# Kernel tuning notes

Measured on AMD Instinct MI355X. Metric: run time of the kernel, lower is better.

## Reference

```python
import jax, jax.numpy as jnp
import numpy as np

N = 100000; E = 1000000; D = 192; FD = 64; L = 6; MLP = 192
TW = 768; NPD = 6; CPD = 7; TEMP = 0.5; NREL = 2; EPS = 1e-5


def _ln(x, g, b):
    mu = jnp.mean(x, axis=-1, keepdims=True)
    var = jnp.mean(jnp.square(x - mu), axis=-1, keepdims=True)
    return (x - mu) * jax.lax.rsqrt(var + EPS) * g + b


def _bn(x, g, b):
    # BatchNorm1d in training mode: batch statistics over the N (node) axis
    mu = jnp.mean(x, axis=0, keepdims=True)
    var = jnp.mean(jnp.square(x - mu), axis=0, keepdims=True)
    return (x - mu) * jax.lax.rsqrt(var + EPS) * g + b


def _rgcn(x, Wrel, Wroot, bias, src, dst, etype):
    # PyG RGCNConv, aggr='mean': out_i = x_i @ Wroot + b + sum_r mean_{j in N_r(i)} x_j @ W_r
    out = x @ Wroot + bias
    for r in range(NREL):
        h = x @ Wrel[r]                                   # [N, D] per-relation transform
        mask = (etype == r)
        msg = jnp.where(mask[:, None], jnp.take(h, src, axis=0), 0.0)  # [E, D]
        agg = jax.ops.segment_sum(msg, dst, num_segments=N)
        cnt = jax.ops.segment_sum(mask.astype(x.dtype), dst, num_segments=N)
        out = out + agg / jnp.maximum(cnt, 1.0)[:, None]
    return out


def _forward(tweet, num_prop, comments_prop,
             Wt, bt, Wn, bnum, Wc, bc,
             Wv, bv, Wo, bo, ln1_g, ln1_b, bn_g, bn_b,
             W1, b1, W2, b2, ln2_g, ln2_b,
             Wrel, Wroot, rgcn_b, Wm1, bm1, Wm2, bm2, Wm3, bm3,
             edge_index, edge_type, labels, train_idx):
    lrelu = jax.nn.leaky_relu  # negative_slope=0.01, same as torch LeakyReLU default
    t = lrelu(tweet @ Wt + bt)
    n = lrelu(num_prop @ Wn + bnum)
    c = lrelu(comments_prop @ Wc + bc)
    x = jnp.concatenate([t, n, c], axis=1)  # [N, D]; seq dim of size 1 is elided
    for i in range(L):
        # MHA over seq_len=1: softmax over a single key is exactly 1, so
        # attn_out = out_proj(v_proj(x)); Q/K projections have zero effect/grad.
        v = x @ Wv[i] + bv[i]
        x = x + (v @ Wo[i] + bo[i])          # dropout in eval mode = identity
        x = _ln(x, ln1_g[i], ln1_b[i])
        x = _bn(x, bn_g[i], bn_b[i])
        f = lrelu(x @ W1[i] + b1[i]) @ W2[i] + b2[i]
        x = x + f
        x = _ln(x, ln2_g[i], ln2_b[i])
    # supervised contrastive loss on first train_idx nodes (train_idx static int)
    feat = x[:train_idx]
    lab = labels[:train_idx]
    fn = feat / jnp.linalg.norm(feat, axis=-1, keepdims=True)
    sim = (fn @ fn.T) / TEMP                              # [T, T]
    ex = jnp.exp(sim)
    match = (lab[:, None] == lab[None, :]).astype(x.dtype)
    closs = jnp.mean(-jnp.log(jnp.sum(match * ex, axis=1) / jnp.sum(ex, axis=1)))
    # two passes through the SAME (shared-weight) RGCN; dropout(p=0.1) eval = identity
    src, dst = edge_index[0], edge_index[1]
    h = _rgcn(x, Wrel, Wroot, rgcn_b, src, dst, edge_type)
    h = _rgcn(h, Wrel, Wroot, rgcn_b, src, dst, edge_type)
    h = lrelu(h @ Wm1 + bm1)
    h = lrelu(h @ Wm2 + bm2)
    logits = h @ Wm3 + bm3                                # [N, 2]
    return logits, closs


def setup_inputs() -> dict:
    key = jax.random.key(0)
    ks = iter(jax.random.split(key, 64))
    f32 = jnp.float32
    def p(*shape):
        fan_in = shape[-2] if len(shape) >= 2 else shape[-1]
        return jax.random.normal(next(ks), shape, f32) * (1.0 / np.sqrt(fan_in))
    inp = {
        'tweet': jax.random.normal(next(ks), (N, TW), f32),
        'num_prop': jax.random.normal(next(ks), (N, NPD), f32),
        'comments_prop': jax.random.normal(next(ks), (N, CPD), f32),
        'Wt': p(TW, FD), 'bt': jnp.zeros((FD,), f32),
        'Wn': p(NPD, FD), 'bnum': jnp.zeros((FD,), f32),
        'Wc': p(CPD, FD), 'bc': jnp.zeros((FD,), f32),
        'Wv': p(L, D, D), 'bv': jnp.zeros((L, D), f32),
        'Wo': p(L, D, D), 'bo': jnp.zeros((L, D), f32),
        'ln1_g': jnp.ones((L, D), f32), 'ln1_b': jnp.zeros((L, D), f32),
        'bn_g': jnp.ones((L, D), f32), 'bn_b': jnp.zeros((L, D), f32),
        'W1': p(L, D, MLP), 'b1': jnp.zeros((L, MLP), f32),
        'W2': p(L, MLP, D), 'b2': jnp.zeros((L, D), f32),
        'ln2_g': jnp.ones((L, D), f32), 'ln2_b': jnp.zeros((L, D), f32),
        'Wrel': p(NREL, D, D), 'Wroot': p(D, D), 'rgcn_b': jnp.zeros((D,), f32),
        'Wm1': p(D, MLP), 'bm1': jnp.zeros((MLP,), f32),
        'Wm2': p(MLP, D), 'bm2': jnp.zeros((D,), f32),
        'Wm3': p(D, 2), 'bm3': jnp.zeros((2,), f32),
        'edge_index': jax.random.randint(next(ks), (2, E), 0, N, jnp.int32),
        'edge_type': jax.random.randint(next(ks), (E,), 0, NREL, jnp.int32),
        'labels': jax.random.randint(next(ks), (N,), 0, 2, jnp.int32),
        'train_idx': 8192,
    }
    return inp


def reference(tweet, num_prop, comments_prop, Wt, bt, Wn, bnum, Wc, bc,
              Wv, bv, Wo, bo, ln1_g, ln1_b, bn_g, bn_b,
              W1, b1, W2, b2, ln2_g, ln2_b,
              Wrel, Wroot, rgcn_b, Wm1, bm1, Wm2, bm2, Wm3, bm3,
              edge_index, edge_type, labels, train_idx):
    return _forward(tweet, num_prop, comments_prop, Wt, bt, Wn, bnum, Wc, bc,
                    Wv, bv, Wo, bo, ln1_g, ln1_b, bn_g, bn_b,
                    W1, b1, W2, b2, ln2_g, ln2_b,
                    Wrel, Wroot, rgcn_b, Wm1, bm1, Wm2, bm2, Wm3, bm3,
                    edge_index, edge_type, labels, train_idx)
```

## Files before the change

kernel.cpp:

```cpp
#include <hip/hip_runtime.h>

#define NN 100000
#define EE 1000000
#define DDIM 192
#define NLAYER 6
#define TRAIN 8192
#define SLOPE 0.01f
#define EPS_LN 1e-5f
#define TOTSEG (2 * NN)
#define SCAN_NB 98

typedef float f32x4 __attribute__((ext_vector_type(4)));
typedef __bf16 bf16x8 __attribute__((ext_vector_type(8)));
typedef unsigned short ushort_t;
typedef unsigned int uint_t;

__device__ __forceinline__ float lrelu(float v) { return v > 0.0f ? v : SLOPE * v; }

__device__ __forceinline__ ushort_t f2bf(float f) {
    union { float f; uint_t u; } v; v.f = f;
    uint_t u = v.u;
    u += 0x7fffu + ((u >> 16) & 1u);
    return (ushort_t)(u >> 16);
}

__device__ __forceinline__ float bf2f(ushort_t b) {
    union { uint_t u; float f; } v; v.u = ((uint_t)b) << 16; return v.f;
}

__device__ __forceinline__ float wave_sum(float s) {
    #pragma unroll
    for (int off = 32; off > 0; off >>= 1) s += __shfl_down(s, off);
    return __shfl(s, 0);
}

__global__ __launch_bounds__(256) void prep_w(
    const float* __restrict__ Wt, const float* __restrict__ Wv,
    const float* __restrict__ Wo, const float* __restrict__ W1,
    const float* __restrict__ W2, const float* __restrict__ Wrel,
    const float* __restrict__ Wroot, const float* __restrict__ Wm1,
    const float* __restrict__ Wm2, ushort_t* __restrict__ WTt,
    ushort_t* __restrict__ WTs, ushort_t* __restrict__ WTg)
{
    const int bid = blockIdx.x;
    if (bid < 29 * 144) {
        const int mat = bid / 144;
        const int o = (bid % 144) * 256 + threadIdx.x;
        const float* src;
        if      (mat <  6) src = Wv   + (size_t)mat * 36864;
        else if (mat < 12) src = Wo   + (size_t)(mat - 6)  * 36864;
        else if (mat < 18) src = W1   + (size_t)(mat - 12) * 36864;
        else if (mat < 24) src = W2   + (size_t)(mat - 18) * 36864;
        else if (mat < 26) src = Wrel + (size_t)(mat - 24) * 36864;
        else if (mat == 26) src = Wroot;
        else if (mat == 27) src = Wm1;
        else                src = Wm2;
        const int m = o / 192, k = o - m * 192;
        const ushort_t b = f2bf(src[(size_t)k * 192 + m]);
        if (mat == 24 || mat == 25)
            WTg[(size_t)m * 576 + 192 + (mat - 24) * 192 + k] = b;
        else if (mat == 26)
            WTg[(size_t)m * 576 + k] = b;
        else
            WTs[(size_t)mat * 36864 + o] = b;
    } else {
        const int o = (bid - 29 * 144) * 256 + threadIdx.x;
        const int m = o / 768, k = o - m * 768;
        WTt[o] = f2bf(Wt[(size_t)k * 64 + m]);
    }
}

template <int NFRAG, bool BIAS, bool RELU>
__global__ __launch_bounds__(256) void gemm_mfma(
    const float* __restrict__ A, const ushort_t* __restrict__ WT,
    const float* __restrict__ bias, float* __restrict__ C,
    int n, int K, int ldc)
{
    __shared__ ushort_t As[128 * 32];
    __shared__ ushort_t Ws[NFRAG * 16 * 32];
    const int tid = threadIdx.x;
    const int lane = tid & 63, w = tid >> 6;
    const int quad = lane >> 4, l15 = lane & 15;
    const int row0 = blockIdx.x * 128;

    f32x4 acc[2][NFRAG];
    #pragma unroll
    for (int m = 0; m < 2; ++m)
        #pragma unroll
        for (int nf = 0; nf < NFRAG; ++nf)
            acc[m][nf] = (f32x4){0.f, 0.f, 0.f, 0.f};

    const int srow = tid >> 1, shalf = tid & 1;
    const bool arow_ok = (row0 + srow) < n;
    const float* aptr = A + (size_t)(row0 + srow) * K + shalf * 16;
    const int ktiles = K >> 5;

    float f[16];
    if (arow_ok) {
        const float4* p = (const float4*)aptr;
        #pragma unroll
        for (int i = 0; i < 4; ++i) {
            const float4 t4 = p[i];
            f[i * 4 + 0] = t4.x; f[i * 4 + 1] = t4.y;
            f[i * 4 + 2] = t4.z; f[i * 4 + 3] = t4.w;
        }
    } else {
        #pragma unroll
        for (int i = 0; i < 16; ++i) f[i] = 0.f;
    }

    for (int t = 0; t < ktiles; ++t) {
        const int k0 = t << 5;
        uint_t u[8];
        #pragma unroll
        for (int i = 0; i < 8; ++i)
            u[i] = (uint_t)f2bf(f[2 * i]) | ((uint_t)f2bf(f[2 * i + 1]) << 16);
        uint4* dsta = (uint4*)&As[srow * 32 + shalf * 16];
        dsta[0] = make_uint4(u[0], u[1], u[2], u[3]);
        dsta[1] = make_uint4(u[4], u[5], u[6], u[7]);

        #pragma unroll
        for (int s = tid; s < NFRAG * 64; s += 256) {
            const int col = s >> 2, part = s & 3;
            *(uint4*)&Ws[col * 32 + part * 8] =
                *(const uint4*)(WT + (size_t)col * K + k0 + part * 8);
        }
        __syncthreads();

        float fn_[16];
        const bool more = (t + 1 < ktiles);
        if (more) {
            if (arow_ok) {
                const float4* p = (const float4*)(aptr + k0 + 32);
                #pragma unroll
                for (int i = 0; i < 4; ++i) {
                    const float4 t4 = p[i];
                    fn_[i * 4 + 0] = t4.x; fn_[i * 4 + 1] = t4.y;
                    fn_[i * 4 + 2] = t4.z; fn_[i * 4 + 3] = t4.w;
                }
            } else {
                #pragma unroll
                for (int i = 0; i < 16; ++i) fn_[i] = 0.f;
            }
        }

        const bf16x8 a0 = *(const bf16x8*)&As[(w * 32 + l15) * 32 + quad * 8];
        const bf16x8 a1 = *(const bf16x8*)&As[(w * 32 + 16 + l15) * 32 + quad * 8];
        #pragma unroll
        for (int nf = 0; nf < NFRAG; ++nf) {
            const bf16x8 b = *(const bf16x8*)&Ws[(nf * 16 + l15) * 32 + quad * 8];
            acc[0][nf] = __builtin_amdgcn_mfma_f32_16x16x32_bf16(a0, b, acc[0][nf], 0, 0, 0);
            acc[1][nf] = __builtin_amdgcn_mfma_f32_16x16x32_bf16(a1, b, acc[1][nf], 0, 0, 0);
        }
        __syncthreads();
        if (more) {
            #pragma unroll
            for (int i = 0; i < 16; ++i) f[i] = fn_[i];
        }
    }

    #pragma unroll
    for (int m = 0; m < 2; ++m) {
        #pragma unroll
        for (int reg = 0; reg < 4; ++reg) {
            const int gr = row0 + w * 32 + m * 16 + quad * 4 + reg;
            if (gr >= n) continue;
            #pragma unroll
            for (int nf = 0; nf < NFRAG; ++nf) {
                const int col = nf * 16 + l15;
                float x = acc[m][nf][reg] + (BIAS ? bias[col] : 0.f);
                if (RELU) x = lrelu(x);
                C[(size_t)gr * ldc + col] = x;
            }
        }
    }
}

template <bool RELU1, bool RELU2, bool RES, bool LNORM, bool BNIN,
          bool BNRES, bool BNSTAT, bool CBF>
__global__ __launch_bounds__(256, 2) void gemm2_mfma(
    const float* __restrict__ A, const ushort_t* __restrict__ wta,
    const float* __restrict__ bias1, const ushort_t* __restrict__ wtb,
    const float* __restrict__ bias2, const float* __restrict__ res,
    float* __restrict__ C, ushort_t* __restrict__ Cbf,
    const float* __restrict__ bns, float* __restrict__ bnacc,
    const float* __restrict__ lg, const float* __restrict__ lb, int n)
{
    constexpr int VST = 200;
    __shared__ ushort_t Vs[128 * VST];
    __shared__ ushort_t Ws[192 * 32];
    ushort_t* As = Vs;
    const int tid = threadIdx.x;
    const int lane = tid & 63, w = tid >> 6;
    const int quad = lane >> 4, l15 = lane & 15;
    const int row0 = blockIdx.x * 128;

    f32x4 acc[2][12];
    #pragma unroll
    for (int m = 0; m < 2; ++m)
        #pragma unroll
        for (int nf = 0; nf < 12; ++nf)
            acc[m][nf] = (f32x4){0.f, 0.f, 0.f, 0.f};

    const int srow = tid >> 1, shalf = tid & 1;
    const bool arow_ok = (row0 + srow) < n;
    const float* aptr = A + (size_t)(row0 + srow) * DDIM + shalf * 16;

    float f[16];
    if (arow_ok) {
        const float4* p = (const float4*)aptr;
        #pragma unroll
        for (int i = 0; i < 4; ++i) {
            const float4 t4 = p[i];
            f[i * 4 + 0] = t4.x; f[i * 4 + 1] = t4.y;
            f[i * 4 + 2] = t4.z; f[i * 4 + 3] = t4.w;
        }
    } else {
        #pragma unroll
        for (int i = 0; i < 16; ++i) f[i] = 0.f;
    }

    #pragma unroll 1
    for (int t = 0; t < 6; ++t) {
        const int k0 = t << 5;
        if (BNIN) {
            const float4* scp = (const float4*)(bns + 2 * DDIM + k0 + shalf * 16);
            const float4* shp = (const float4*)(bns + 3 * DDIM + k0 + shalf * 16);
            #pragma unroll
            for (int i = 0; i < 4; ++i) {
                const float4 sc = scp[i], sh = shp[i];
                f[i * 4 + 0] = fmaf(f[i * 4 + 0], sc.x, sh.x);
                f[i * 4 + 1] = fmaf(f[i * 4 + 1], sc.y, sh.y);
                f[i * 4 + 2] = fmaf(f[i * 4 + 2], sc.z, sh.z);
                f[i * 4 + 3] = fmaf(f[i * 4 + 3], sc.w, sh.w);
            }
        }
        uint_t u[8];
        #pragma unroll
        for (int i = 0; i < 8; ++i)
            u[i] = (uint_t)f2bf(f[2 * i]) | ((uint_t)f2bf(f[2 * i + 1]) << 16);
        uint4* dsta = (uint4*)&As[srow * 32 + shalf * 16];
        dsta[0] = make_uint4(u[0], u[1], u[2], u[3]);
        dsta[1] = make_uint4(u[4], u[5], u[6], u[7]);

        #pragma unroll
        for (int s = tid; s < 768; s += 256) {
            const int col = s >> 2, part = s & 3;
            *(uint4*)&Ws[col * 32 + part * 8] =
                *(const uint4*)(wta + (size_t)col * DDIM + k0 + part * 8);
        }
        __syncthreads();

        float fn_[16];
        const bool more = (t < 5);
        if (more) {
            if (arow_ok) {
                const float4* p = (const float4*)(aptr + k0 + 32);
                #pragma unroll
                for (int i = 0; i < 4; ++i) {
                    const float4 t4 = p[i];
                    fn_[i * 4 + 0] = t4.x; fn_[i * 4 + 1] = t4.y;
                    fn_[i * 4 + 2] = t4.z; fn_[i * 4 + 3] = t4.w;
                }
            } else {
                #pragma unroll
                for (int i = 0; i < 16; ++i) fn_[i] = 0.f;
            }
        }

        const bf16x8 a0 = *(const bf16x8*)&As[(w * 32 + l15) * 32 + quad * 8];
        const bf16x8 a1 = *(const bf16x8*)&As[(w * 32 + 16 + l15) * 32 + quad * 8];
        #pragma unroll
        for (int nf = 0; nf < 12; ++nf) {
            const bf16x8 b = *(const bf16x8*)&Ws[(nf * 16 + l15) * 32 + quad * 8];
            acc[0][nf] = __builtin_amdgcn_mfma_f32_16x16x32_bf16(a0, b, acc[0][nf], 0, 0, 0);
            acc[1][nf] = __builtin_amdgcn_mfma_f32_16x16x32_bf16(a1, b, acc[1][nf], 0, 0, 0);
        }
        __syncthreads();
        if (more) {
            #pragma unroll
            for (int i = 0; i < 16; ++i) f[i] = fn_[i];
        }
    }

    {
        float b1r[12];
        #pragma unroll
        for (int nf = 0; nf < 12; ++nf) b1r[nf] = bias1[nf * 16 + l15];
        #pragma unroll
        for (int m = 0; m < 2; ++m) {
            #pragma unroll
            for (int reg = 0; reg < 4; ++reg) {
                ushort_t* vrow = &Vs[(w * 32 + m * 16 + quad * 4 + reg) * VST + l15];
                #pragma unroll
                for (int nf = 0; nf < 12; ++nf) {
                    float x = acc[m][nf][reg] + b1r[nf];
                    if (RELU1) x = lrelu(x);
                    vrow[nf * 16] = f2bf(x);
                    acc[m][nf][reg] = 0.f;
                }
            }
        }
    }
    __syncthreads();

    #pragma unroll 1
    for (int t = 0; t < 6; ++t) {
        const int k0 = t << 5;
        #pragma unroll
        for (int s = tid; s < 768; s += 256) {
            const int col = s >> 2, part = s & 3;
            *(uint4*)&Ws[col * 32 + part * 8] =
                *(const uint4*)(wtb + (size_t)col * DDIM + k0 + part * 8);
        }
        __syncthreads();
        const bf16x8 a0 = *(const bf16x8*)&Vs[(w * 32 + l15) * VST + k0 + quad * 8];
        const bf16x8 a1 = *(const bf16x8*)&Vs[(w * 32 + 16 + l15) * VST + k0 + quad * 8];
        #pragma unroll
        for (int nf = 0; nf < 12; ++nf) {
            const bf16x8 b = *(const bf16x8*)&Ws[(nf * 16 + l15) * 32 + quad * 8];
            acc[0][nf] = __builtin_amdgcn_mfma_f32_16x16x32_bf16(a0, b, acc[0][nf], 0, 0, 0);
            acc[1][nf] = __builtin_amdgcn_mfma_f32_16x16x32_bf16(a1, b, acc[1][nf], 0, 0, 0);
        }
        __syncthreads();
    }

    int   col[12];
    float bia[12];
    #pragma unroll
    for (int nf = 0; nf < 12; ++nf) {
        col[nf] = nf * 16 + l15;
        bia[nf] = bias2[col[nf]];
    }
    float rsc[12], rsh[12];
    if (BNRES) {
        #pragma unroll
        for (int nf = 0; nf < 12; ++nf) {
            rsc[nf] = bns[2 * DDIM + col[nf]];
            rsh[nf] = bns[3 * DDIM + col[nf]];
        }
    }
    float cs[12], cs2[12];
    if (BNSTAT) {
        #pragma unroll
        for (int nf = 0; nf < 12; ++nf) { cs[nf] = 0.f; cs2[nf] = 0.f; }
    }
    #pragma unroll
    for (int m = 0; m < 2; ++m) {
        #pragma unroll
        for (int reg = 0; reg < 4; ++reg) {
            const int gr = row0 + w * 32 + m * 16 + quad * 4 + reg;
            const bool ok = gr < n;
            float v[12];
            #pragma unroll
            for (int nf = 0; nf < 12; ++nf) {
                float x = acc[m][nf][reg] + bia[nf];
                if (RES) {
                    float r = ok ? res[(size_t)gr * DDIM + col[nf]] : 0.f;
                    if (BNRES) r = fmaf(r, rsc[nf], rsh[nf]);
                    x += r;
                }
                v[nf] = x;
            }
            if (LNORM) {
                float s = 0.f, s2 = 0.f;
                #pragma unroll
                for (int nf = 0; nf < 12; ++nf) { s += v[nf]; s2 = fmaf(v[nf], v[nf], s2); }
                #pragma unroll
                for (int off = 1; off < 16; off <<= 1) {
                    s  += __shfl_xor(s, off);
                    s2 += __shfl_xor(s2, off);
                }
                const float mu = s * (1.0f / DDIM);
                const float var = s2 * (1.0f / DDIM) - mu * mu;
                const float rs = rsqrtf(var + EPS_LN);
                #pragma unroll
                for (int nf = 0; nf < 12; ++nf)
                    v[nf] = fmaf((v[nf] - mu) * rs, lg[col[nf]], lb[col[nf]]);
            }
            #pragma unroll
            for (int nf = 0; nf < 12; ++nf) {
                float x = v[nf];
                if (RELU2) x = lrelu(x);
                if (BNSTAT) {
                    const float xa = ok ? x : 0.f;
                    cs[nf] += xa;
                    cs2[nf] = fmaf(xa, xa, cs2[nf]);
                }
                if (ok) {
                    C[(size_t)gr * DDIM + col[nf]] = x;
                    if (CBF) Cbf[(size_t)gr * DDIM + col[nf]] = f2bf(x);
                }
            }
        }
    }
    if (BNSTAT) {
        float* bsA = (float*)Ws;
        float* bsB = bsA + 4 * 192;
        #pragma unroll
        for (int nf = 0; nf < 12; ++nf) {
            cs[nf]  += __shfl_xor(cs[nf], 16);  cs[nf]  += __shfl_xor(cs[nf], 32);
            cs2[nf] += __shfl_xor(cs2[nf], 16); cs2[nf] += __shfl_xor(cs2[nf], 32);
        }
        if (quad == 0) {
            #pragma unroll
            for (int nf = 0; nf < 12; ++nf) {
                bsA[w * 192 + col[nf]] = cs[nf];
                bsB[w * 192 + col[nf]] = cs2[nf];
            }
        }
        __syncthreads();
        if (tid < DDIM) {
            const float s  = bsA[tid] + bsA[192 + tid] + bsA[384 + tid] + bsA[576 + tid];
            const float s2 = bsB[tid] + bsB[192 + tid] + bsB[384 + tid] + bsB[576 + tid];
            atomicAdd(&bnacc[tid], s);
            atomicAdd(&bnacc[DDIM + tid], s2);
        }
    }
}

template <bool CBF>
__global__ __launch_bounds__(256) void gemm_cat(
    const ushort_t* __restrict__ A1, const ushort_t* __restrict__ A2,
    const ushort_t* __restrict__ WT, const float* __restrict__ bias,
    float* __restrict__ C, ushort_t* __restrict__ Cbf, int n)
{
    __shared__ ushort_t As[128 * 32];
    __shared__ ushort_t Ws[192 * 32];
    const int tid = threadIdx.x;
    const int lane = tid & 63, w = tid >> 6;
    const int quad = lane >> 4, l15 = lane & 15;
    const int row0 = blockIdx.x * 128;

    f32x4 acc[2][12];
    #pragma unroll
    for (int m = 0; m < 2; ++m)
        #pragma unroll
        for (int nf = 0; nf < 12; ++nf)
            acc[m][nf] = (f32x4){0.f, 0.f, 0.f, 0.f};

    const int srow = tid >> 1, shalf = tid & 1;
    const bool arow_ok = (row0 + srow) < n;
    const ushort_t* a1p = A1 + (size_t)(row0 + srow) * 192 + shalf * 16;
    const ushort_t* a2p = A2 + (size_t)(row0 + srow) * 384 + shalf * 16;

    uint_t u[8];
    if (arow_ok) {
        const uint4* p = (const uint4*)a1p;
        const uint4 q0 = p[0], q1 = p[1];
        u[0] = q0.x; u[1] = q0.y; u[2] = q0.z; u[3] = q0.w;
        u[4] = q1.x; u[5] = q1.y; u[6] = q1.z; u[7] = q1.w;
    } else {
        #pragma unroll
        for (int i = 0; i < 8; ++i) u[i] = 0u;
    }

    #pragma unroll 1
    for (int t = 0; t < 18; ++t) {
        uint4* dsta = (uint4*)&As[srow * 32 + shalf * 16];
        dsta[0] = make_uint4(u[0], u[1], u[2], u[3]);
        dsta[1] = make_uint4(u[4], u[5], u[6], u[7]);

        #pragma unroll
        for (int s = tid; s < 768; s += 256) {
            const int col = s >> 2, part = s & 3;
            *(uint4*)&Ws[col * 32 + part * 8] =
                *(const uint4*)(WT + (size_t)col * 576 + t * 32 + part * 8);
        }
        __syncthreads();

        uint_t un[8];
        const bool more = (t < 17);
        if (more) {
            if (arow_ok) {
                const int tn = t + 1;
                const ushort_t* np = (tn < 6) ? (a1p + tn * 32)
                                              : (a2p + (tn - 6) * 32);
                const uint4* p = (const uint4*)np;
                const uint4 q0 = p[0], q1 = p[1];
                un[0] = q0.x; un[1] = q0.y; un[2] = q0.z; un[3] = q0.w;
                un[4] = q1.x; un[5] = q1.y; un[6] = q1.z; un[7] = q1.w;
            } else {
                #pragma unroll
                for (int i = 0; i < 8; ++i) un[i] = 0u;
            }
        }

        const bf16x8 a0 = *(const bf16x8*)&As[(w * 32 + l15) * 32 + quad * 8];
        const bf16x8 a1 = *(const bf16x8*)&As[(w * 32 + 16 + l15) * 32 + quad * 8];
        #pragma unroll
        for (int nf = 0; nf < 12; ++nf) {
            const bf16x8 b = *(const bf16x8*)&Ws[(nf * 16 + l15) * 32 + quad * 8];
            acc[0][nf] = __builtin_amdgcn_mfma_f32_16x16x32_bf16(a0, b, acc[0][nf], 0, 0, 0);
            acc[1][nf] = __builtin_amdgcn_mfma_f32_16x16x32_bf16(a1, b, acc[1][nf], 0, 0, 0);
        }
        __syncthreads();
        if (more) {
            #pragma unroll
            for (int i = 0; i < 8; ++i) u[i] = un[i];
        }
    }

    #pragma unroll
    for (int m = 0; m < 2; ++m) {
        #pragma unroll
        for (int reg = 0; reg < 4; ++reg) {
            const int gr = row0 + w * 32 + m * 16 + quad * 4 + reg;
            if (gr >= n) continue;
            #pragma unroll
            for (int nf = 0; nf < 12; ++nf) {
                const int col = nf * 16 + l15;
                const float x = acc[m][nf][reg] + bias[col];
                C[(size_t)gr * DDIM + col] = x;
                if (CBF) Cbf[(size_t)gr * DDIM + col] = f2bf(x);
            }
        }
    }
}

__global__ __launch_bounds__(256) void embed_nc_k(
    const float* __restrict__ np_, const float* __restrict__ cp,
    const float* __restrict__ Wn, const float* __restrict__ bnum,
    const float* __restrict__ Wc, const float* __restrict__ bc,
    float* __restrict__ x)
{
    const int idx = blockIdx.x * 256 + threadIdx.x;
    if (idx >= NN * 128) return;
    const int node = idx >> 7;
    const int c = idx & 127;
    float acc;
    if (c < 64) {
        acc = bnum[c];
        #pragma unroll
        for (int k = 0; k < 6; ++k) acc = fmaf(np_[node * 6 + k], Wn[k * 64 + c], acc);
    } else {
        const int cc = c - 64;
        acc = bc[cc];
        #pragma unroll
        for (int k = 0; k < 7; ++k) acc = fmaf(cp[node * 7 + k], Wc[k * 64 + cc], acc);
    }
    x[(size_t)node * DDIM + 64 + c] = lrelu(acc);
}

__global__ __launch_bounds__(192) void bn_fin_k(float* __restrict__ bns,
    const float* __restrict__ g, const float* __restrict__ b)
{
    const int j = threadIdx.x;
    const float invN = 1.0f / (float)NN;
    const float mu = bns[j] * invN;
    const float var = bns[DDIM + j] * invN - mu * mu;
    const float sc = g[j] * rsqrtf(var + EPS_LN);
    bns[2 * DDIM + j] = sc;
    bns[3 * DDIM + j] = fmaf(-mu, sc, b[j]);
}

__global__ __launch_bounds__(256) void fnorm_k(const float* __restrict__ x,
                                               ushort_t* __restrict__ fnb)
{
    const int wave = threadIdx.x >> 6, lane = threadIdx.x & 63;
    const int row = blockIdx.x * 4 + wave;
    if (row >= TRAIN) return;
    const float* xr = x + (size_t)row * DDIM;
    const float v0 = xr[lane], v1 = xr[lane + 64], v2 = xr[lane + 128];
    const float q = wave_sum(v0 * v0 + v1 * v1 + v2 * v2);
    const float inv = 1.0f / sqrtf(q);
    ushort_t* fr = fnb + (size_t)row * DDIM;
    fr[lane]       = f2bf(v0 * inv);
    fr[lane + 64]  = f2bf(v1 * inv);
    fr[lane + 128] = f2bf(v2 * inv);
}

__global__ __launch_bounds__(256) void sim_mfma(const ushort_t* __restrict__ fnb,
    const int* __restrict__ lab, float* __restrict__ row_ex, float* __restrict__ row_mt)
{
    __shared__ ushort_t Ai[128 * 32];
    __shared__ ushort_t Bj[128 * 32];
    __shared__ int Li[128], Lj[128];
    const int tid = threadIdx.x, lane = tid & 63, w = tid >> 6;
    const int quad = lane >> 4, l15 = lane & 15;
    const int i0 = blockIdx.x * 128, j0 = blockIdx.y * 128;
    if (tid < 128) Li[tid] = lab[i0 + tid];
    else           Lj[tid - 128] = lab[j0 + tid - 128];
    const int iw = (w >> 1) * 64, jw = (w & 1) * 64;

    f32x4 acc[4][4];
    #pragma unroll
    for (int m = 0; m < 4; ++m)
        #pragma unroll
        for (int nf = 0; nf < 4; ++nf)
            acc[m][nf] = (f32x4){0.f, 0.f, 0.f, 0.f};

    for (int k0 = 0; k0 < DDIM; k0 += 32) {
        #pragma unroll
        for (int s = tid; s < 512; s += 256) {
            const int row = s >> 2, part = s & 3;
            *(uint4*)&Ai[row * 32 + part * 8] =
                *(const uint4*)(fnb + (size_t)(i0 + row) * DDIM + k0 + part * 8);
            *(uint4*)&Bj[row * 32 + part * 8] =
                *(const uint4*)(fnb + (size_t)(j0 + row) * DDIM + k0 + part * 8);
        }
        __syncthreads();
        bf16x8 a[4], b[4];
        #pragma unroll
        for (int m = 0; m < 4; ++m)
            a[m] = *(const bf16x8*)&Ai[(iw + m * 16 + l15) * 32 + quad * 8];
        #pragma unroll
        for (int nf = 0; nf < 4; ++nf)
            b[nf] = *(const bf16x8*)&Bj[(jw + nf * 16 + l15) * 32 + quad * 8];
        #pragma unroll
        for (int m = 0; m < 4; ++m)
            #pragma unroll
            for (int nf = 0; nf < 4; ++nf)
                acc[m][nf] = __builtin_amdgcn_mfma_f32_16x16x32_bf16(a[m], b[nf], acc[m][nf], 0, 0, 0);
        __syncthreads();
    }

    int lj[4];
    #pragma unroll
    for (int nf = 0; nf < 4; ++nf) lj[nf] = Lj[jw + nf * 16 + l15];
    #pragma unroll
    for (int m = 0; m < 4; ++m) {
        #pragma unroll
        for (int reg = 0; reg < 4; ++reg) {
            const int rl = iw + m * 16 + quad * 4 + reg;
            const int li = Li[rl];
            float se = 0.f, sm = 0.f;
            #pragma unroll
            for (int nf = 0; nf < 4; ++nf) {
                const float e = __expf(acc[m][nf][reg] * 2.0f);
                se += e;
                if (li == lj[nf]) sm += e;
            }
            #pragma unroll
            for (int off = 1; off < 16; off <<= 1) {
                se += __shfl_xor(se, off);
                sm += __shfl_xor(sm, off);
            }
            if (l15 == 0) {
                atomicAdd(&row_ex[i0 + rl], se);
                atomicAdd(&row_mt[i0 + rl], sm);
            }
        }
    }
}

__global__ __launch_bounds__(256) void closs_k(const float* __restrict__ ex,
    const float* __restrict__ mt, float* __restrict__ out)
{
    float s = 0.f;
    for (int i = threadIdx.x; i < TRAIN; i += 256) s += -logf(mt[i] / ex[i]);
    s = wave_sum(s);
    __shared__ float red[4];
    const int wave = threadIdx.x >> 6, lane = threadIdx.x & 63;
    if (lane == 0) red[wave] = s;
    __syncthreads();
    if (threadIdx.x == 0) out[0] = (red[0] + red[1] + red[2] + red[3]) / (float)TRAIN;
}

__global__ __launch_bounds__(256) void cnt_i_k(const int* __restrict__ dst,
    const int* __restrict__ ety, int* __restrict__ cnti)
{
    const int e = blockIdx.x * 256 + threadIdx.x;
    if (e >= EE) return;
    atomicAdd(&cnti[(size_t)ety[e] * NN + dst[e]], 1);
}

__global__ __launch_bounds__(256) void part_k(const int* __restrict__ cnti,
                                              int* __restrict__ part)
{
    __shared__ int sh[256];
    const int tid = threadIdx.x;
    const int i0 = blockIdx.x * 2048 + tid * 8;
    int s = 0;
    #pragma unroll
    for (int j = 0; j < 8; ++j) {
        const int i = i0 + j;
        s += (i < TOTSEG) ? cnti[i] : 0;
    }
    sh[tid] = s;
    __syncthreads();
    #pragma unroll
    for (int off = 128; off > 0; off >>= 1) {
        if (tid < off) sh[tid] += sh[tid + off];
        __syncthreads();
    }
    if (tid == 0) part[blockIdx.x] = sh[0];
}

__global__ __launch_bounds__(128) void scanp_k(int* __restrict__ part)
{
    __shared__ int sh[128];
    const int tid = threadIdx.x;
    const int v = (tid < SCAN_NB) ? part[tid] : 0;
    sh[tid] = v;
    __syncthreads();
    #pragma unroll
    for (int off = 1; off < 128; off <<= 1) {
        const int t = (tid >= off) ? sh[tid - off] : 0;
        __syncthreads();
        sh[tid] += t;
        __syncthreads();
    }
    if (tid < SCAN_NB) part[tid] = sh[tid] - v;
}

__global__ __launch_bounds__(256) void offs_k(const int* __restrict__ cnti,
    const int* __restrict__ part, int* __restrict__ offs)
{
    __shared__ int sh[256];
    const int tid = threadIdx.x;
    const int i0 = blockIdx.x * 2048 + tid * 8;
    int v[8];
    int loc = 0;
    #pragma unroll
    for (int j = 0; j < 8; ++j) {
        const int i = i0 + j;
        v[j] = (i < TOTSEG) ? cnti[i] : 0;
        loc += v[j];
    }
    sh[tid] = loc;
    __syncthreads();
    #pragma unroll
    for (int off = 1; off < 256; off <<= 1) {
        const int t = (tid >= off) ? sh[tid - off] : 0;
        __syncthreads();
        sh[tid] += t;
        __syncthreads();
    }
    int pre = part[blockIdx.x] + sh[tid] - loc;
    #pragma unroll
    for (int j = 0; j < 8; ++j) {
        const int i = i0 + j;
        if (i < TOTSEG) offs[i] = pre;
        pre += v[j];
    }
}

__global__ __launch_bounds__(256) void fill_k(const int* __restrict__ src,
    const int* __restrict__ dst, const int* __restrict__ ety,
    int* __restrict__ offs, int* __restrict__ elist)
{
    const int e = blockIdx.x * 256 + threadIdx.x;
    if (e >= EE) return;
    const int pos = atomicAdd(&offs[(size_t)ety[e] * NN + dst[e]], 1);
    elist[pos] = src[e];
}

__global__ __launch_bounds__(256) void gather_bf_k(const ushort_t* __restrict__ xb,
    const int* __restrict__ elist, const int* __restrict__ offs,
    const int* __restrict__ cnti, ushort_t* __restrict__ aggb)
{
    const int wave = threadIdx.x >> 6, lane = threadIdx.x & 63;
    const int d = blockIdx.x * 4 + wave;
    if (d >= NN) return;
    #pragma unroll
    for (int r = 0; r < 2; ++r) {
        const int seg = r * NN + d;
        const int end = offs[seg];
        const int c = cnti[seg];
        float a0 = 0.f, a1 = 0.f, a2 = 0.f;
        for (int e = end - c; e < end; ++e) {
            const int s = elist[e];
            const ushort_t* xr = xb + (size_t)s * DDIM;
            a0 += bf2f(xr[lane]); a1 += bf2f(xr[lane + 64]); a2 += bf2f(xr[lane + 128]);
        }
        const float inv = 1.0f / (float)max(c, 1);
        ushort_t* ar = aggb + (size_t)d * 384 + r * DDIM;
        ar[lane]       = f2bf(a0 * inv);
        ar[lane + 64]  = f2bf(a1 * inv);
        ar[lane + 128] = f2bf(a2 * inv);
    }
}

__global__ __launch_bounds__(256) void logits_k(const float* __restrict__ h,
    const float* __restrict__ Wm3, const float* __restrict__ bm3, float* __restrict__ out)
{
    const int wave = threadIdx.x >> 6, lane = threadIdx.x & 63;
    const int row = blockIdx.x * 4 + wave;
    if (row >= NN) return;
    const float* hr = h + (size_t)row * DDIM;
    float s0 = 0.f, s1 = 0.f;
    #pragma unroll
    for (int p = 0; p < 3; ++p) {
        const int k = lane + p * 64;
        const float v = hr[k];
        s0 = fmaf(v, Wm3[k * 2 + 0], s0);
        s1 = fmaf(v, Wm3[k * 2 + 1], s1);
    }
    #pragma unroll
    for (int off = 32; off > 0; off >>= 1) {
        s0 += __shfl_down(s0, off);
        s1 += __shfl_down(s1, off);
    }
    if (lane == 0) {
        out[(size_t)row * 2 + 0] = s0 + bm3[0];
        out[(size_t)row * 2 + 1] = s1 + bm3[1];
    }
}

extern "C" void kernel_launch(void* const* d_in, const int* in_sizes, int n_in,
                              void* d_out, int out_size, void* d_ws, size_t ws_size,
                              hipStream_t stream)
{
    const float* tweet   = (const float*)d_in[0];
    const float* np_     = (const float*)d_in[1];
    const float* cp      = (const float*)d_in[2];
    const float* Wt      = (const float*)d_in[3];
    const float* bt      = (const float*)d_in[4];
    const float* Wn      = (const float*)d_in[5];
    const float* bnum    = (const float*)d_in[6];
    const float* Wc      = (const float*)d_in[7];
    const float* bc      = (const float*)d_in[8];
    const float* Wv      = (const float*)d_in[9];
    const float* bv      = (const float*)d_in[10];
    const float* Wo      = (const float*)d_in[11];
    const float* bo      = (const float*)d_in[12];
    const float* ln1g    = (const float*)d_in[13];
    const float* ln1b    = (const float*)d_in[14];
    const float* bng     = (const float*)d_in[15];
    const float* bnb     = (const float*)d_in[16];
    const float* W1      = (const float*)d_in[17];
    const float* b1      = (const float*)d_in[18];
    const float* W2      = (const float*)d_in[19];
    const float* b2      = (const float*)d_in[20];
    const float* ln2g    = (const float*)d_in[21];
    const float* ln2b    = (const float*)d_in[22];
    const float* Wrel    = (const float*)d_in[23];
    const float* Wroot   = (const float*)d_in[24];
    const float* rgcnb   = (const float*)d_in[25];
    const float* Wm1     = (const float*)d_in[26];
    const float* bm1     = (const float*)d_in[27];
    const float* Wm2     = (const float*)d_in[28];
    const float* bm2     = (const float*)d_in[29];
    const float* Wm3     = (const float*)d_in[30];
    const float* bm3     = (const float*)d_in[31];
    const int*   eidx    = (const int*)d_in[32];
    const int*   esrc    = eidx;
    const int*   edst    = eidx + EE;
    const int*   ety     = (const int*)d_in[33];
    const int*   labels  = (const int*)d_in[34];
    float* out = (float*)d_out;

    float* ws = (float*)d_ws;
    const size_t ND = (size_t)NN * DDIM;
    float* B0    = ws;
    float* B1    = B0 + ND;
    float* B2    = B1 + ND;
    float* B3    = B2 + ND;
    float* ROWEX = B3 + ND;
    float* ROWMT = ROWEX + TRAIN;
    float* BNS   = ROWMT + TRAIN;
    int*   CNTI  = (int*)(BNS + 4 * DDIM);
    int*   OFFS  = CNTI + 2 * NN;
    int*   ELIST = OFFS + 2 * NN;
    int*   PART  = ELIST + EE;
    ushort_t* FNb = (ushort_t*)(PART + 128);
    ushort_t* WTt = FNb + (size_t)TRAIN * DDIM;
    ushort_t* WTs = WTt + 49152;
    ushort_t* WTv    = WTs;
    ushort_t* WTo    = WTs + (size_t)6  * 36864;
    ushort_t* WT1    = WTs + (size_t)12 * 36864;
    ushort_t* WT2    = WTs + (size_t)18 * 36864;
    ushort_t* WTm1   = WTs + (size_t)27 * 36864;
    ushort_t* WTm2   = WTs + (size_t)28 * 36864;
    ushort_t* XBF  = (ushort_t*)B3;
    ushort_t* WTg  = (ushort_t*)B3 + ND;
    ushort_t* AGGB = (ushort_t*)B2;

    const int gx = (NN + 127) / 128;
    const dim3 blk(256);

    prep_w<<<29 * 144 + 192, blk, 0, stream>>>(Wt, Wv, Wo, W1, W2, Wrel, Wroot, Wm1, Wm2, WTt, WTs, WTg);

    hipMemsetAsync(CNTI, 0, 2 * NN * sizeof(int), stream);
    cnt_i_k<<<(EE + 255) / 256, blk, 0, stream>>>(edst, ety, CNTI);
    part_k<<<SCAN_NB, blk, 0, stream>>>(CNTI, PART);
    scanp_k<<<1, 128, 0, stream>>>(PART);
    offs_k<<<SCAN_NB, blk, 0, stream>>>(CNTI, PART, OFFS);
    fill_k<<<(EE + 255) / 256, blk, 0, stream>>>(esrc, edst, ety, OFFS, ELIST);

    gemm_mfma<4, true, true><<<gx, blk, 0, stream>>>(tweet, WTt, bt, B0, NN, 768, DDIM);
    embed_nc_k<<<(NN * 128 + 255) / 256, blk, 0, stream>>>(np_, cp, Wn, bnum, Wc, bc, B0);

    for (int i = 0; i < NLAYER; ++i) {
        const size_t wo = (size_t)i * 36864;
        hipMemsetAsync(BNS, 0, 2 * DDIM * sizeof(float), stream);
        gemm2_mfma<false, false, true, true, false, false, true, false><<<gx, blk, 0, stream>>>(
            B0, WTv + wo, bv + i * DDIM, WTo + wo, bo + i * DDIM,
            B0, B2, nullptr, nullptr, BNS, ln1g + i * DDIM, ln1b + i * DDIM, NN);
        bn_fin_k<<<1, dim3(192), 0, stream>>>(BNS, bng + i * DDIM, bnb + i * DDIM);
        if (i < NLAYER - 1)
            gemm2_mfma<true, false, true, true, true, true, false, false><<<gx, blk, 0, stream>>>(
                B2, WT1 + wo, b1 + i * DDIM, WT2 + wo, b2 + i * DDIM,
                B2, B0, nullptr, BNS, nullptr, ln2g + i * DDIM, ln2b + i * DDIM, NN);
        else
            gemm2_mfma<true, false, true, true, true, true, false, true><<<gx, blk, 0, stream>>>(
                B2, WT1 + wo, b1 + i * DDIM, WT2 + wo, b2 + i * DDIM,
                B2, B0, XBF, BNS, nullptr, ln2g + i * DDIM, ln2b + i * DDIM, NN);
    }

    hipMemsetAsync(ROWEX, 0, 2 * TRAIN * sizeof(float), stream);
    fnorm_k<<<TRAIN / 4, blk, 0, stream>>>(B0, FNb);
    sim_mfma<<<dim3(TRAIN / 128, TRAIN / 128), blk, 0, stream>>>(FNb, labels, ROWEX, ROWMT);
    closs_k<<<1, blk, 0, stream>>>(ROWEX, ROWMT, out + 2 * (size_t)NN);

    gather_bf_k<<<(NN + 3) / 4, blk, 0, stream>>>(XBF, ELIST, OFFS, CNTI, AGGB);
    gemm_cat<true><<<gx, blk, 0, stream>>>(XBF, AGGB, WTg, rgcnb, B0, XBF, NN);

    gather_bf_k<<<(NN + 3) / 4, blk, 0, stream>>>(XBF, ELIST, OFFS, CNTI, AGGB);
    gemm_cat<false><<<gx, blk, 0, stream>>>(XBF, AGGB, WTg, rgcnb, B0, nullptr, NN);

    gemm2_mfma<true, true, false, false, false, false, false, false><<<gx, blk, 0, stream>>>(
        B0, WTm1, bm1, WTm2, bm2, nullptr, B2, nullptr,
        nullptr, nullptr, nullptr, nullptr, NN);
    logits_k<<<(NN + 3) / 4, blk, 0, stream>>>(B2, Wm3, bm3, out);
}
```

Measured before the change: 2.172 ms.

## Store layer intermediates in bf16, fold BN finalize into GEMM, vectorize gather

```diff
diff --git a/kernel.cpp b/kernel.cpp
--- a/kernel.cpp
+++ b/kernel.cpp
@@ -176,25 +176,39 @@
     }
 }
 
-template <bool RELU1, bool RELU2, bool RES, bool LNORM, bool BNIN,
-          bool BNRES, bool BNSTAT, bool CBF>
+template <bool ABF, bool RELU1, bool RELU2, bool RES, bool LNORM, bool BN,
+          bool BNSTAT, bool CF32, bool CBF>
 __global__ __launch_bounds__(256, 2) void gemm2_mfma(
-    const float* __restrict__ A, const ushort_t* __restrict__ wta,
+    const void* __restrict__ Ain, const ushort_t* __restrict__ wta,
     const float* __restrict__ bias1, const ushort_t* __restrict__ wtb,
-    const float* __restrict__ bias2, const float* __restrict__ res,
+    const float* __restrict__ bias2, const void* __restrict__ resin,
     float* __restrict__ C, ushort_t* __restrict__ Cbf,
-    const float* __restrict__ bns, float* __restrict__ bnacc,
+    const float* __restrict__ bnsum, const float* __restrict__ bng,
+    const float* __restrict__ bnb, float* __restrict__ bnacc,
     const float* __restrict__ lg, const float* __restrict__ lb, int n)
 {
     constexpr int VST = 200;
     __shared__ ushort_t Vs[128 * VST];
     __shared__ ushort_t Ws[192 * 32];
+    __shared__ float scs[DDIM], shs[DDIM];
     ushort_t* As = Vs;
     const int tid = threadIdx.x;
     const int lane = tid & 63, w = tid >> 6;
     const int quad = lane >> 4, l15 = lane & 15;
     const int row0 = blockIdx.x * 128;
 
+    if constexpr (BN) {
+        const float invN = 1.0f / (float)NN;
+        for (int j = tid; j < DDIM; j += 256) {
+            const float mu = bnsum[j] * invN;
+            const float var = bnsum[DDIM + j] * invN - mu * mu;
+            const float sc = bng[j] * rsqrtf(var + EPS_LN);
+            scs[j] = sc;
+            shs[j] = fmaf(-mu, sc, bnb[j]);
+        }
+        __syncthreads();
+    }
+
     f32x4 acc[2][12];
     #pragma unroll
     for (int m = 0; m < 2; ++m)
@@ -204,44 +218,67 @@
 
     const int srow = tid >> 1, shalf = tid & 1;
     const bool arow_ok = (row0 + srow) < n;
-    const float* aptr = A + (size_t)(row0 + srow) * DDIM + shalf * 16;
+    const float*    aF = (const float*)Ain + (size_t)(row0 + srow) * DDIM + shalf * 16;
+    const ushort_t* aB = (const ushort_t*)Ain + (size_t)(row0 + srow) * DDIM + shalf * 16;
 
     float f[16];
-    if (arow_ok) {
-        const float4* p = (const float4*)aptr;
-        #pragma unroll
-        for (int i = 0; i < 4; ++i) {
-            const float4 t4 = p[i];
-            f[i * 4 + 0] = t4.x; f[i * 4 + 1] = t4.y;
-            f[i * 4 + 2] = t4.z; f[i * 4 + 3] = t4.w;
+    uint4 ub[2];
+
+    if constexpr (!ABF) {
+        if (arow_ok) {
+            const float4* p = (const float4*)aF;
+            #pragma unroll
+            for (int i = 0; i < 4; ++i) {
+                const float4 t4 = p[i];
+                f[i * 4 + 0] = t4.x; f[i * 4 + 1] = t4.y;
+                f[i * 4 + 2] = t4.z; f[i * 4 + 3] = t4.w;
+            }
+        } else {
+            #pragma unroll
+            for (int i = 0; i < 16; ++i) f[i] = 0.f;
         }
     } else {
-        #pragma unroll
-        for (int i = 0; i < 16; ++i) f[i] = 0.f;
+        if (arow_ok) {
+            const uint4* p = (const uint4*)aB;
+            ub[0] = p[0]; ub[1] = p[1];
+        } else {
+            ub[0] = make_uint4(0, 0, 0, 0); ub[1] = make_uint4(0, 0, 0, 0);
+        }
     }
 
     #pragma unroll 1
     for (int t = 0; t < 6; ++t) {
         const int k0 = t << 5;
-        if (BNIN) {
-            const float4* scp = (const float4*)(bns + 2 * DDIM + k0 + shalf * 16);
-            const float4* shp = (const float4*)(bns + 3 * DDIM + k0 + shalf * 16);
+        uint4* dsta = (uint4*)&As[srow * 32 + shalf * 16];
+        if constexpr (!ABF) {
+            uint_t u[8];
+            #pragma unroll
+            for (int i = 0; i < 8; ++i)
+                u[i] = (uint_t)f2bf(f[2 * i]) | ((uint_t)f2bf(f[2 * i + 1]) << 16);
+            dsta[0] = make_uint4(u[0], u[1], u[2], u[3]);
+            dsta[1] = make_uint4(u[4], u[5], u[6], u[7]);
+        } else if constexpr (BN) {
+            const float4* scp = (const float4*)&scs[k0 + shalf * 16];
+            const float4* shp = (const float4*)&shs[k0 + shalf * 16];
+            const uint_t* uw = (const uint_t*)ub;
+            uint_t u[8];
             #pragma unroll
             for (int i = 0; i < 4; ++i) {
                 const float4 sc = scp[i], sh = shp[i];
-                f[i * 4 + 0] = fmaf(f[i * 4 + 0], sc.x, sh.x);
-                f[i * 4 + 1] = fmaf(f[i * 4 + 1], sc.y, sh.y);
-                f[i * 4 + 2] = fmaf(f[i * 4 + 2], sc.z, sh.z);
-                f[i * 4 + 3] = fmaf(f[i * 4 + 3], sc.w, sh.w);
-            }
-        }
-        uint_t u[8];
-        #pragma unroll
-        for (int i = 0; i < 8; ++i)
-            u[i] = (uint_t)f2bf(f[2 * i]) | ((uint_t)f2bf(f[2 * i + 1]) << 16);
-        uint4* dsta = (uint4*)&As[srow * 32 + shalf * 16];
-        dsta[0] = make_uint4(u[0], u[1], u[2], u[3]);
-        dsta[1] = make_uint4(u[4], u[5], u[6], u[7]);
+                float x0 = bf2f((ushort_t)(uw[2 * i] & 0xffffu));
+                float x1 = bf2f((ushort_t)(uw[2 * i] >> 16));
+                float x2 = bf2f((ushort_t)(uw[2 * i + 1] & 0xffffu));
+                float x3 = bf2f((ushort_t)(uw[2 * i + 1] >> 16));
+                x0 = fmaf(x0, sc.x, sh.x); x1 = fmaf(x1, sc.y, sh.y);
+                x2 = fmaf(x2, sc.z, sh.z); x3 = fmaf(x3, sc.w, sh.w);
+                u[2 * i]     = (uint_t)f2bf(x0) | ((uint_t)f2bf(x1) << 16);
+                u[2 * i + 1] = (uint_t)f2bf(x2) | ((uint_t)f2bf(x3) << 16);
+            }
+            dsta[0] = make_uint4(u[0], u[1], u[2], u[3]);
+            dsta[1] = make_uint4(u[4], u[5], u[6], u[7]);
+        } else {
+            dsta[0] = ub[0]; dsta[1] = ub[1];
+        }
 
         #pragma unroll
         for (int s = tid; s < 768; s += 256) {
@@ -252,19 +289,29 @@
         __syncthreads();
 
         float fn_[16];
+        uint4 ubn[2];
         const bool more = (t < 5);
         if (more) {
-            if (arow_ok) {
-                const float4* p = (const float4*)(aptr + k0 + 32);
-                #pragma unroll
-                for (int i = 0; i < 4; ++i) {
-                    const float4 t4 = p[i];
-                    fn_[i * 4 + 0] = t4.x; fn_[i * 4 + 1] = t4.y;
-                    fn_[i * 4 + 2] = t4.z; fn_[i * 4 + 3] = t4.w;
+            if constexpr (!ABF) {
+                if (arow_ok) {
+                    const float4* p = (const float4*)(aF + k0 + 32);
+                    #pragma unroll
+                    for (int i = 0; i < 4; ++i) {
+                        const float4 t4 = p[i];
+                        fn_[i * 4 + 0] = t4.x; fn_[i * 4 + 1] = t4.y;
+                        fn_[i * 4 + 2] = t4.z; fn_[i * 4 + 3] = t4.w;
+                    }
+                } else {
+                    #pragma unroll
+                    for (int i = 0; i < 16; ++i) fn_[i] = 0.f;
                 }
             } else {
-                #pragma unroll
-                for (int i = 0; i < 16; ++i) fn_[i] = 0.f;
+                if (arow_ok) {
+                    const uint4* p = (const uint4*)(aB + k0 + 32);
+                    ubn[0] = p[0]; ubn[1] = p[1];
+                } else {
+                    ubn[0] = make_uint4(0, 0, 0, 0); ubn[1] = make_uint4(0, 0, 0, 0);
+                }
             }
         }
 
@@ -278,8 +325,12 @@
         }
         __syncthreads();
         if (more) {
-            #pragma unroll
-            for (int i = 0; i < 16; ++i) f[i] = fn_[i];
+            if constexpr (!ABF) {
+                #pragma unroll
+                for (int i = 0; i < 16; ++i) f[i] = fn_[i];
+            } else {
+                ub[0] = ubn[0]; ub[1] = ubn[1];
+            }
         }
     }
 
@@ -333,15 +384,15 @@
         bia[nf] = bias2[col[nf]];
     }
     float rsc[12], rsh[12];
-    if (BNRES) {
+    if constexpr (BN && RES) {
         #pragma unroll
         for (int nf = 0; nf < 12; ++nf) {
-            rsc[nf] = bns[2 * DDIM + col[nf]];
-            rsh[nf] = bns[3 * DDIM + col[nf]];
+            rsc[nf] = scs[col[nf]];
+            rsh[nf] = shs[col[nf]];
         }
     }
     float cs[12], cs2[12];
-    if (BNSTAT) {
+    if constexpr (BNSTAT) {
         #pragma unroll
         for (int nf = 0; nf < 12; ++nf) { cs[nf] = 0.f; cs2[nf] = 0.f; }
     }
@@ -355,14 +406,18 @@
             #pragma unroll
             for (int nf = 0; nf < 12; ++nf) {
                 float x = acc[m][nf][reg] + bia[nf];
-                if (RES) {
-                    float r = ok ? res[(size_t)gr * DDIM + col[nf]] : 0.f;
-                    if (BNRES) r = fmaf(r, rsc[nf], rsh[nf]);
+                if constexpr (RES) {
+                    float r;
+                    if constexpr (ABF)
+                        r = ok ? bf2f(((const ushort_t*)resin)[(size_t)gr * DDIM + col[nf]]) : 0.f;
+                    else
+                        r = ok ? ((const float*)resin)[(size_t)gr * DDIM + col[nf]] : 0.f;
+                    if constexpr (BN) r = fmaf(r, rsc[nf], rsh[nf]);
                     x += r;
                 }
                 v[nf] = x;
             }
-            if (LNORM) {
+            if constexpr (LNORM) {
                 float s = 0.f, s2 = 0.f;
                 #pragma unroll
                 for (int nf = 0; nf < 12; ++nf) { s += v[nf]; s2 = fmaf(v[nf], v[nf], s2); }
@@ -382,19 +437,19 @@
             for (int nf = 0; nf < 12; ++nf) {
                 float x = v[nf];
                 if (RELU2) x = lrelu(x);
-                if (BNSTAT) {
+                if constexpr (BNSTAT) {
                     const float xa = ok ? x : 0.f;
                     cs[nf] += xa;
                     cs2[nf] = fmaf(xa, xa, cs2[nf]);
                 }
                 if (ok) {
-                    C[(size_t)gr * DDIM + col[nf]] = x;
-                    if (CBF) Cbf[(size_t)gr * DDIM + col[nf]] = f2bf(x);
+                    if constexpr (CF32) C[(size_t)gr * DDIM + col[nf]] = x;
+                    if constexpr (CBF)  Cbf[(size_t)gr * DDIM + col[nf]] = f2bf(x);
                 }
             }
         }
     }
-    if (BNSTAT) {
+    if constexpr (BNSTAT) {
         float* bsA = (float*)Ws;
         float* bsB = bsA + 4 * 192;
         #pragma unroll
@@ -419,11 +474,10 @@
     }
 }
 
-template <bool CBF>
 __global__ __launch_bounds__(256) void gemm_cat(
     const ushort_t* __restrict__ A1, const ushort_t* __restrict__ A2,
     const ushort_t* __restrict__ WT, const float* __restrict__ bias,
-    float* __restrict__ C, ushort_t* __restrict__ Cbf, int n)
+    ushort_t* __restrict__ Cbf, int n)
 {
     __shared__ ushort_t As[128 * 32];
     __shared__ ushort_t Ws[192 * 32];
@@ -444,22 +498,19 @@
     const ushort_t* a1p = A1 + (size_t)(row0 + srow) * 192 + shalf * 16;
     const ushort_t* a2p = A2 + (size_t)(row0 + srow) * 384 + shalf * 16;
 
-    uint_t u[8];
+    uint4 u0, u1;
     if (arow_ok) {
         const uint4* p = (const uint4*)a1p;
-        const uint4 q0 = p[0], q1 = p[1];
-        u[0] = q0.x; u[1] = q0.y; u[2] = q0.z; u[3] = q0.w;
-        u[4] = q1.x; u[5] = q1.y; u[6] = q1.z; u[7] = q1.w;
+        u0 = p[0]; u1 = p[1];
     } else {
-        #pragma unroll
-        for (int i = 0; i < 8; ++i) u[i] = 0u;
+        u0 = make_uint4(0, 0, 0, 0); u1 = make_uint4(0, 0, 0, 0);
     }
 
     #pragma unroll 1
     for (int t = 0; t < 18; ++t) {
         uint4* dsta = (uint4*)&As[srow * 32 + shalf * 16];
-        dsta[0] = make_uint4(u[0], u[1], u[2], u[3]);
-        dsta[1] = make_uint4(u[4], u[5], u[6], u[7]);
+        dsta[0] = u0;
+        dsta[1] = u1;
 
         #pragma unroll
         for (int s = tid; s < 768; s += 256) {
@@ -469,7 +520,7 @@
         }
         __syncthreads();
 
-        uint_t un[8];
+        uint4 un0, un1;
         const bool more = (t < 17);
         if (more) {
             if (arow_ok) {
@@ -477,12 +528,9 @@
                 const ushort_t* np = (tn < 6) ? (a1p + tn * 32)
                                               : (a2p + (tn - 6) * 32);
                 const uint4* p = (const uint4*)np;
-                const uint4 q0 = p[0], q1 = p[1];
-                un[0] = q0.x; un[1] = q0.y; un[2] = q0.z; un[3] = q0.w;
-                un[4] = q1.x; un[5] = q1.y; un[6] = q1.z; un[7] = q1.w;
+                un0 = p[0]; un1 = p[1];
             } else {
-                #pragma unroll
-                for (int i = 0; i < 8; ++i) un[i] = 0u;
+                un0 = make_uint4(0, 0, 0, 0); un1 = make_uint4(0, 0, 0, 0);
             }
         }
 
@@ -495,10 +543,7 @@
             acc[1][nf] = __builtin_amdgcn_mfma_f32_16x16x32_bf16(a1, b, acc[1][nf], 0, 0, 0);
         }
         __syncthreads();
-        if (more) {
-            #pragma unroll
-            for (int i = 0; i < 8; ++i) u[i] = un[i];
-        }
+        if (more) { u0 = un0; u1 = un1; }
     }
 
     #pragma unroll
@@ -510,9 +555,7 @@
             #pragma unroll
             for (int nf = 0; nf < 12; ++nf) {
                 const int col = nf * 16 + l15;
-                const float x = acc[m][nf][reg] + bias[col];
-                C[(size_t)gr * DDIM + col] = x;
-                if (CBF) Cbf[(size_t)gr * DDIM + col] = f2bf(x);
+                Cbf[(size_t)gr * DDIM + col] = f2bf(acc[m][nf][reg] + bias[col]);
             }
         }
     }
@@ -540,18 +583,6 @@
         for (int k = 0; k < 7; ++k) acc = fmaf(cp[node * 7 + k], Wc[k * 64 + cc], acc);
     }
     x[(size_t)node * DDIM + 64 + c] = lrelu(acc);
-}
-
-__global__ __launch_bounds__(192) void bn_fin_k(float* __restrict__ bns,
-    const float* __restrict__ g, const float* __restrict__ b)
-{
-    const int j = threadIdx.x;
-    const float invN = 1.0f / (float)NN;
-    const float mu = bns[j] * invN;
-    const float var = bns[DDIM + j] * invN - mu * mu;
-    const float sc = g[j] * rsqrtf(var + EPS_LN);
-    bns[2 * DDIM + j] = sc;
-    bns[3 * DDIM + j] = fmaf(-mu, sc, b[j]);
 }
 
 __global__ __launch_bounds__(256) void fnorm_k(const float* __restrict__ x,
@@ -753,22 +784,42 @@
     const int wave = threadIdx.x >> 6, lane = threadIdx.x & 63;
     const int d = blockIdx.x * 4 + wave;
     if (d >= NN) return;
+    const bool lo = lane < 32;
     #pragma unroll
     for (int r = 0; r < 2; ++r) {
         const int seg = r * NN + d;
         const int end = offs[seg];
         const int c = cnti[seg];
-        float a0 = 0.f, a1 = 0.f, a2 = 0.f;
-        for (int e = end - c; e < end; ++e) {
-            const int s = elist[e];
-            const ushort_t* xr = xb + (size_t)s * DDIM;
-            a0 += bf2f(xr[lane]); a1 += bf2f(xr[lane + 64]); a2 += bf2f(xr[lane + 128]);
+        float a0 = 0.f, a1 = 0.f, b0 = 0.f, b1 = 0.f;
+        int e = end - c;
+        for (; e + 1 < end; e += 2) {
+            const int s0 = elist[e], s1 = elist[e + 1];
+            const uint_t* r0 = (const uint_t*)(xb + (size_t)s0 * DDIM);
+            const uint_t* r1 = (const uint_t*)(xb + (size_t)s1 * DDIM);
+            const uint_t x0 = r0[lane], x1 = r1[lane];
+            uint_t y0 = 0u, y1 = 0u;
+            if (lo) { y0 = r0[64 + lane]; y1 = r1[64 + lane]; }
+            a0 += bf2f((ushort_t)(x0 & 0xffffu)) + bf2f((ushort_t)(x1 & 0xffffu));
+            a1 += bf2f((ushort_t)(x0 >> 16))     + bf2f((ushort_t)(x1 >> 16));
+            b0 += bf2f((ushort_t)(y0 & 0xffffu)) + bf2f((ushort_t)(y1 & 0xffffu));
+            b1 += bf2f((ushort_t)(y0 >> 16))     + bf2f((ushort_t)(y1 >> 16));
+        }
+        if (e < end) {
+            const int s0 = elist[e];
+            const uint_t* r0 = (const uint_t*)(xb + (size_t)s0 * DDIM);
+            const uint_t x0 = r0[lane];
+            uint_t y0 = 0u;
+            if (lo) y0 = r0[64 + lane];
+            a0 += bf2f((ushort_t)(x0 & 0xffffu));
+            a1 += bf2f((ushort_t)(x0 >> 16));
+            b0 += bf2f((ushort_t)(y0 & 0xffffu));
+            b1 += bf2f((ushort_t)(y0 >> 16));
         }
         const float inv = 1.0f / (float)max(c, 1);
-        ushort_t* ar = aggb + (size_t)d * 384 + r * DDIM;
-        ar[lane]       = f2bf(a0 * inv);
-        ar[lane + 64]  = f2bf(a1 * inv);
-        ar[lane + 128] = f2bf(a2 * inv);
+        uint_t* ar = (uint_t*)(aggb + (size_t)d * 384 + r * DDIM);
+        ar[lane] = (uint_t)f2bf(a0 * inv) | ((uint_t)f2bf(a1 * inv) << 16);
+        if (lo)
+            ar[64 + lane] = (uint_t)f2bf(b0 * inv) | ((uint_t)f2bf(b1 * inv) << 16);
     }
 }
 
@@ -850,7 +901,7 @@
     float* ROWEX = B3 + ND;
     float* ROWMT = ROWEX + TRAIN;
     float* BNS   = ROWMT + TRAIN;
-    int*   CNTI  = (int*)(BNS + 4 * DDIM);
+    int*   CNTI  = (int*)(BNS + 12 * DDIM);
     int*   OFFS  = CNTI + 2 * NN;
     int*   ELIST = OFFS + 2 * NN;
     int*   PART  = ELIST + EE;
@@ -865,6 +916,7 @@
     ushort_t* WTm2   = WTs + (size_t)28 * 36864;
     ushort_t* XBF  = (ushort_t*)B3;
     ushort_t* WTg  = (ushort_t*)B3 + ND;
+    ushort_t* X1BF = (ushort_t*)B2;
     ushort_t* AGGB = (ushort_t*)B2;
 
     const int gx = (NN + 127) / 128;
@@ -882,21 +934,27 @@
     gemm_mfma<4, true, true><<<gx, blk, 0, stream>>>(tweet, WTt, bt, B0, NN, 768, DDIM);
     embed_nc_k<<<(NN * 128 + 255) / 256, blk, 0, stream>>>(np_, cp, Wn, bnum, Wc, bc, B0);
 
+    hipMemsetAsync(BNS, 0, 12 * DDIM * sizeof(float), stream);
     for (int i = 0; i < NLAYER; ++i) {
         const size_t wo = (size_t)i * 36864;
-        hipMemsetAsync(BNS, 0, 2 * DDIM * sizeof(float), stream);
-        gemm2_mfma<false, false, true, true, false, false, true, false><<<gx, blk, 0, stream>>>(
-            B0, WTv + wo, bv + i * DDIM, WTo + wo, bo + i * DDIM,
-            B0, B2, nullptr, nullptr, BNS, ln1g + i * DDIM, ln1b + i * DDIM, NN);
-        bn_fin_k<<<1, dim3(192), 0, stream>>>(BNS, bng + i * DDIM, bnb + i * DDIM);
+        float* bnacc_i = BNS + (size_t)i * 2 * DDIM;
+        gemm2_mfma<false, false, false, true, true, false, true, false, true>
+            <<<gx, blk, 0, stream>>>(
+            B0, WTv + wo, bv + i * DDIM, WTo + wo, bo + i * DDIM, B0,
+            nullptr, X1BF, nullptr, nullptr, nullptr, bnacc_i,
+            ln1g + i * DDIM, ln1b + i * DDIM, NN);
         if (i < NLAYER - 1)
-            gemm2_mfma<true, false, true, true, true, true, false, false><<<gx, blk, 0, stream>>>(
-                B2, WT1 + wo, b1 + i * DDIM, WT2 + wo, b2 + i * DDIM,
-                B2, B0, nullptr, BNS, nullptr, ln2g + i * DDIM, ln2b + i * DDIM, NN);
+            gemm2_mfma<true, true, false, true, true, true, false, true, false>
+                <<<gx, blk, 0, stream>>>(
+                X1BF, WT1 + wo, b1 + i * DDIM, WT2 + wo, b2 + i * DDIM, X1BF,
+                B0, nullptr, bnacc_i, bng + i * DDIM, bnb + i * DDIM, nullptr,
+                ln2g + i * DDIM, ln2b + i * DDIM, NN);
         else
-            gemm2_mfma<true, false, true, true, true, true, false, true><<<gx, blk, 0, stream>>>(
-                B2, WT1 + wo, b1 + i * DDIM, WT2 + wo, b2 + i * DDIM,
-                B2, B0, XBF, BNS, nullptr, ln2g + i * DDIM, ln2b + i * DDIM, NN);
+            gemm2_mfma<true, true, false, true, true, true, false, true, true>
+                <<<gx, blk, 0, stream>>>(
+                X1BF, WT1 + wo, b1 + i * DDIM, WT2 + wo, b2 + i * DDIM, X1BF,
+                B0, XBF, bnacc_i, bng + i * DDIM, bnb + i * DDIM, nullptr,
+                ln2g + i * DDIM, ln2b + i * DDIM, NN);
     }
 
     hipMemsetAsync(ROWEX, 0, 2 * TRAIN * sizeof(float), stream);
@@ -905,13 +963,14 @@
     closs_k<<<1, blk, 0, stream>>>(ROWEX, ROWMT, out + 2 * (size_t)NN);
 
     gather_bf_k<<<(NN + 3) / 4, blk, 0, stream>>>(XBF, ELIST, OFFS, CNTI, AGGB);
-    gemm_cat<true><<<gx, blk, 0, stream>>>(XBF, AGGB, WTg, rgcnb, B0, XBF, NN);
+    gemm_cat<<<gx, blk, 0, stream>>>(XBF, AGGB, WTg, rgcnb, XBF, NN);
 
     gather_bf_k<<<(NN + 3) / 4, blk, 0, stream>>>(XBF, ELIST, OFFS, CNTI, AGGB);
-    gemm_cat<false><<<gx, blk, 0, stream>>>(XBF, AGGB, WTg, rgcnb, B0, nullptr, NN);
-
-    gemm2_mfma<true, true, false, false, false, false, false, false><<<gx, blk, 0, stream>>>(
-        B0, WTm1, bm1, WTm2, bm2, nullptr, B2, nullptr,
-        nullptr, nullptr, nullptr, nullptr, NN);
+    gemm_cat<<<gx, blk, 0, stream>>>(XBF, AGGB, WTg, rgcnb, XBF, NN);
+
+    gemm2_mfma<true, true, true, false, false, false, false, true, false>
+        <<<gx, blk, 0, stream>>>(
+        XBF, WTm1, bm1, WTm2, bm2, nullptr, B2, nullptr,
+        nullptr, nullptr, nullptr, nullptr, nullptr, nullptr, NN);
     logits_k<<<(NN + 3) / 4, blk, 0, stream>>>(B2, Wm3, bm3, out);
 }
```

After: 2.105 ms. -3.1%, faster.
